# Kernel tuning notes

Measured on AMD Instinct MI355X. Metric: run time of the kernel, lower is better.

## Reference

```python
import jax, jax.numpy as jnp
import numpy as np

N = 50000      # nodes
E = 500000     # edges (includes N self-loops)
DIN = 512
DOUT = 256
NEG_SLOPE = 0.01  # torch nn.LeakyReLU default


def setup_inputs() -> dict:
    key = jax.random.key(0)
    k1, k2, k3, k4, k5 = jax.random.split(key, 5)
    x = jax.random.normal(k1, (N, DIN), dtype=jnp.float32)
    # xavier_normal_ with gain=1.414
    std_W = 1.414 * np.sqrt(2.0 / (DIN + DOUT))
    W = jax.random.normal(k2, (DIN, DOUT), dtype=jnp.float32) * std_W
    std_a = 1.414 * np.sqrt(2.0 / (1 + 2 * DOUT))
    a = jax.random.normal(k3, (2 * DOUT,), dtype=jnp.float32) * std_a
    # first N edges are self-loops so every row-sum is nonzero
    loops = jnp.arange(N, dtype=jnp.int32)
    edge_src = jnp.concatenate([loops, jax.random.randint(k4, (E - N,), 0, N, dtype=jnp.int32)])
    edge_dst = jnp.concatenate([loops, jax.random.randint(k5, (E - N,), 0, N, dtype=jnp.int32)])
    return {"x": x, "W": W, "a": a, "edge_src": edge_src, "edge_dst": edge_dst}


def reference(x, W, a, edge_src, edge_dst):
    n = x.shape[0]
    d = W.shape[1]
    h = x @ W  # [N, DOUT]
    # a . [h_src ; h_dst] decomposed per-node, then gathered per-edge
    s_src = h @ a[:d]   # [N]
    s_dst = h @ a[d:]   # [N]
    score = s_src[edge_src] + s_dst[edge_dst]          # [E]
    e = jnp.exp(-jax.nn.leaky_relu(score, NEG_SLOPE))  # [E]
    # sparse softmax denominator: spmm(edge, e, ones) == segment sum over src
    e_rowsum = jax.ops.segment_sum(e, edge_src, num_segments=n)            # [N]
    # numerator: spmm(edge, e, h) == sum_j e_ij * h_j per row i
    h_prime = jax.ops.segment_sum(e[:, None] * h[edge_dst], edge_src, num_segments=n)  # [N, DOUT]
    h_prime = h_prime / e_rowsum[:, None]
    return jax.nn.elu(h_prime)  # concat=True branch
```

## Files before the change

kernel.cpp:

```cpp
#include <hip/hip_runtime.h>
#include <math.h>

#define DIN 512
#define DOUT 256
#define NEG_SLOPE 0.01f

typedef __attribute__((ext_vector_type(8))) short bf16x8;
typedef __attribute__((ext_vector_type(4))) float f32x4;
typedef __attribute__((ext_vector_type(4))) unsigned int u32x4;

__device__ __forceinline__ unsigned short f2bf(float f) {
    unsigned int u = __float_as_uint(f);
    unsigned int r = (u + 0x7FFFu + ((u >> 16) & 1u)) >> 16;
    return (unsigned short)r;
}
__device__ __forceinline__ float bf2f(unsigned short u) {
    return __uint_as_float(((unsigned int)u) << 16);
}
__device__ __forceinline__ unsigned int cvtpk(float lo, float hi) {
    unsigned int r;
    asm("v_cvt_pk_bf16_f32 %0, %1, %2" : "=v"(r) : "v"(lo), "v"(hi));
    return r;
}
__device__ __forceinline__ void gload16(const void* g, void* l) {
    __builtin_amdgcn_global_load_lds(
        (const __attribute__((address_space(1))) void*)g,
        (__attribute__((address_space(3))) void*)l, 16, 0, 0);
}

__global__ void prep(const float* __restrict__ W, unsigned short* __restrict__ Bp,
                     int* __restrict__ deg, float* __restrict__ s_src,
                     float* __restrict__ s_dst, int N) {
    int t = blockIdx.x * blockDim.x + threadIdx.x;
    if (t < (DIN / 32) * (DOUT / 16) * 64) {
        int lane = t & 63;
        int cg = (t >> 6) & 15;
        int ks = t >> 10;
        int l15 = lane & 15, g = lane >> 4;
        int col = cg * 16 + l15;
        int k0 = ks * 32 + g * 8;
        ushort4 lo, hi;
        lo.x = f2bf(W[(size_t)(k0 + 0) * DOUT + col]);
        lo.y = f2bf(W[(size_t)(k0 + 1) * DOUT + col]);
        lo.z = f2bf(W[(size_t)(k0 + 2) * DOUT + col]);
        lo.w = f2bf(W[(size_t)(k0 + 3) * DOUT + col]);
        hi.x = f2bf(W[(size_t)(k0 + 4) * DOUT + col]);
        hi.y = f2bf(W[(size_t)(k0 + 5) * DOUT + col]);
        hi.z = f2bf(W[(size_t)(k0 + 6) * DOUT + col]);
        hi.w = f2bf(W[(size_t)(k0 + 7) * DOUT + col]);
        *(ushort4*)(Bp + (size_t)t * 8) = lo;
        *(ushort4*)(Bp + (size_t)t * 8 + 4) = hi;
    }
    if (t < N) { deg[t] = 0; s_src[t] = 0.f; s_dst[t] = 0.f; }
}

__global__ __launch_bounds__(64, 3) void gemm_k(const float* __restrict__ x,
                                                const unsigned short* __restrict__ Bp,
                                                unsigned short* __restrict__ hb,
                                                const float* __restrict__ av,
                                                float* __restrict__ s_src,
                                                float* __restrict__ s_dst, int M) {
    __shared__ unsigned char As[16384];
    const int lane = threadIdx.x;
    const int l15 = lane & 15;
    const int g = lane >> 4;
    const int m0 = blockIdx.x * 32;
    const int half = blockIdx.y;

    auto stage = [&](int bb, int ks) {
#pragma unroll
        for (int it = 0; it < 4; ++it) {
            int s = it * 64 + lane;
            int row = s >> 3;
            int slot = s & 7;
            int q = slot ^ (row & 7);
            int rg = min(m0 + row, M - 1);
            const float* src = x + (size_t)rg * DIN + ks * 32 + q * 4;
            gload16(src, As + bb * 4096 + it * 1024);
        }
    };

    const unsigned short* pB = Bp + ((size_t)(half * 8) * 64 + lane) * 8;
    f32x4 acc[2][8] = {};
    bf16x8 bB[2][8];

    stage(0, 0);
    stage(1, 1);
#pragma unroll
    for (int cg = 0; cg < 8; ++cg)
        bB[0][cg] = *(const bf16x8*)(pB + (size_t)cg * 512);

#pragma unroll
    for (int ks = 0; ks < 16; ++ks) {
        if (ks < 14) stage((ks + 2) & 3, ks + 2);
        if (ks < 15) {
            const unsigned short* pBn = pB + (size_t)(ks + 1) * 16 * 512;
#pragma unroll
            for (int cg = 0; cg < 8; ++cg)
                bB[(ks + 1) & 1][cg] = *(const bf16x8*)(pBn + (size_t)cg * 512);
        }
        __builtin_amdgcn_sched_barrier(0);
        if (ks < 14)      asm volatile("s_waitcnt vmcnt(24)");
        else if (ks == 14) asm volatile("s_waitcnt vmcnt(20)");
        else               asm volatile("s_waitcnt vmcnt(16)");
        __builtin_amdgcn_sched_barrier(0);
        const unsigned char* Ab = As + (ks & 3) * 4096;
        const int rr0 = l15, rr1 = l15 + 16;
        f32x4 v0 = *(const f32x4*)(Ab + rr0 * 128 + (((2 * g) ^ (rr0 & 7)) << 4));
        f32x4 v1 = *(const f32x4*)(Ab + rr0 * 128 + (((2 * g + 1) ^ (rr0 & 7)) << 4));
        f32x4 w0 = *(const f32x4*)(Ab + rr1 * 128 + (((2 * g) ^ (rr1 & 7)) << 4));
        f32x4 w1 = *(const f32x4*)(Ab + rr1 * 128 + (((2 * g + 1) ^ (rr1 & 7)) << 4));
        u32x4 p;
        p.x = cvtpk(v0.x, v0.y); p.y = cvtpk(v0.z, v0.w);
        p.z = cvtpk(v1.x, v1.y); p.w = cvtpk(v1.z, v1.w);
        bf16x8 af0 = *(bf16x8*)&p;
        u32x4 q;
        q.x = cvtpk(w0.x, w0.y); q.y = cvtpk(w0.z, w0.w);
        q.z = cvtpk(w1.x, w1.y); q.w = cvtpk(w1.z, w1.w);
        bf16x8 af1 = *(bf16x8*)&q;
#pragma unroll
        for (int cg = 0; cg < 8; ++cg) {
            acc[0][cg] = __builtin_amdgcn_mfma_f32_16x16x32_bf16(af0, bB[ks & 1][cg], acc[0][cg], 0, 0, 0);
            acc[1][cg] = __builtin_amdgcn_mfma_f32_16x16x32_bf16(af1, bB[ks & 1][cg], acc[1][cg], 0, 0, 0);
        }
    }

    float as_[8], ad_[8];
#pragma unroll
    for (int cg = 0; cg < 8; ++cg) {
        int col = half * 128 + cg * 16 + l15;
        as_[cg] = av[col];
        ad_[cg] = av[DOUT + col];
    }
#pragma unroll
    for (int rf = 0; rf < 2; ++rf) {
#pragma unroll
        for (int j = 0; j < 4; ++j) {
            int row = m0 + rf * 16 + g * 4 + j;
            float ps = 0.f, pd = 0.f;
#pragma unroll
            for (int cg = 0; cg < 8; ++cg) {
                float v = acc[rf][cg][j];
                ps += v * as_[cg];
                pd += v * ad_[cg];
            }
#pragma unroll
            for (int off = 1; off < 16; off <<= 1) {
                ps += __shfl_xor(ps, off);
                pd += __shfl_xor(pd, off);
            }
            if (row < M) {
#pragma unroll
                for (int cg = 0; cg < 8; ++cg)
                    hb[(size_t)row * DOUT + half * 128 + cg * 16 + l15] = f2bf(acc[rf][cg][j]);
                if (l15 == 0) {
                    atomicAdd(&s_src[row], ps);
                    atomicAdd(&s_dst[row], pd);
                }
            }
        }
    }
}

__global__ void hist_k(const int* __restrict__ src, int* __restrict__ deg, int E) {
    int i = (blockIdx.x * blockDim.x + threadIdx.x) * 4;
    if (i + 3 < E) {
        int4 v = *(const int4*)(src + i);
        atomicAdd(&deg[v.x], 1);
        atomicAdd(&deg[v.y], 1);
        atomicAdd(&deg[v.z], 1);
        atomicAdd(&deg[v.w], 1);
    } else {
        for (int j = i; j < E; ++j) atomicAdd(&deg[src[j]], 1);
    }
}

__global__ __launch_bounds__(256) void block_sum(const int* __restrict__ deg, int* __restrict__ bsum, int N) {
    __shared__ int wsum[4];
    int b = blockIdx.x, t = threadIdx.x;
    int idx = b * 1024 + t * 4;
    int s = 0;
    if (idx + 3 < N) {
        int4 v = *(const int4*)(deg + idx);
        s = v.x + v.y + v.z + v.w;
    } else {
        for (int i = 0; i < 4; i++) if (idx + i < N) s += deg[idx + i];
    }
#pragma unroll
    for (int off = 32; off > 0; off >>= 1) s += __shfl_xor(s, off);
    if ((t & 63) == 0) wsum[t >> 6] = s;
    __syncthreads();
    if (t == 0) bsum[b] = wsum[0] + wsum[1] + wsum[2] + wsum[3];
}

__global__ __launch_bounds__(256) void scan_blk(const int* __restrict__ deg, const int* __restrict__ bsum,
                                                int* __restrict__ rowptr, int* __restrict__ cursor,
                                                int N, int nb, int E) {
    __shared__ int wsum[4];
    __shared__ int boff_s;
    int b = blockIdx.x, t = threadIdx.x;
    if (t < 64) {
        int v = (t < b && t < nb) ? bsum[t] : 0;
#pragma unroll
        for (int off = 32; off > 0; off >>= 1) v += __shfl_xor(v, off);
        if (t == 0) boff_s = v;
    }
    if (b == 0 && t == 0) rowptr[N] = E;
    int idx = b * 1024 + t * 4;
    int v0 = 0, v1 = 0, v2 = 0, v3 = 0;
    if (idx + 3 < N) {
        int4 v = *(const int4*)(deg + idx);
        v0 = v.x; v1 = v.y; v2 = v.z; v3 = v.w;
    } else if (idx < N) {
        v0 = deg[idx];
        if (idx + 1 < N) v1 = deg[idx + 1];
        if (idx + 2 < N) v2 = deg[idx + 2];
    }
    int s = v0 + v1 + v2 + v3;
    int lane = t & 63, wid = t >> 6;
    int x = s;
#pragma unroll
    for (int off = 1; off < 64; off <<= 1) {
        int y = __shfl_up(x, off);
        if (lane >= off) x += y;
    }
    if (lane == 63) wsum[wid] = x;
    __syncthreads();
    int add = boff_s;
    for (int ww = 0; ww < wid; ++ww) add += wsum[ww];
    int e0 = add + x - s;
    int e1 = e0 + v0, e2 = e1 + v1, e3 = e2 + v2;
    if (idx < N)     { rowptr[idx] = e0;     cursor[idx] = e0; }
    if (idx + 1 < N) { rowptr[idx + 1] = e1; cursor[idx + 1] = e1; }
    if (idx + 2 < N) { rowptr[idx + 2] = e2; cursor[idx + 2] = e2; }
    if (idx + 3 < N) { rowptr[idx + 3] = e3; cursor[idx + 3] = e3; }
}

__global__ void edge_k(const int* __restrict__ src, const int* __restrict__ dst,
                       const float* __restrict__ s_src, const float* __restrict__ s_dst,
                       int* __restrict__ cursor, int2* __restrict__ csr, int E) {
    int i = blockIdx.x * blockDim.x + threadIdx.x;
    if (i >= E) return;
    int s = src[i], d = dst[i];
    float sc = s_src[s] + s_dst[d];
    float lrv = sc > 0.f ? sc : NEG_SLOPE * sc;
    float ev = __expf(-lrv);
    int pos = atomicAdd(&cursor[s], 1);
    csr[pos] = make_int2(d, __float_as_int(ev));
}

__global__ __launch_bounds__(256) void gather_k(const unsigned short* __restrict__ hb,
                                                const int* __restrict__ rowptr,
                                                const int2* __restrict__ csr,
                                                float* __restrict__ out, int N) {
    int gt = blockIdx.x * blockDim.x + threadIdx.x;
    int w = gt >> 6;
    int lane = threadIdx.x & 63;
    if (w >= N) return;
    int s0 = rowptr[w], s1 = rowptr[w + 1];
    float a0 = 0.f, a1 = 0.f, a2 = 0.f, a3 = 0.f, rs = 0.f;
    for (int base = s0; base < s1; base += 64) {
        int cnt = min(64, s1 - base);
        int dv = 0; float ev = 0.f;
        if (lane < cnt) {
            int2 p = csr[base + lane];
            dv = p.x; ev = __int_as_float(p.y);
        }
        int jj = 0;
        for (; jj + 4 <= cnt; jj += 4) {
            int d0 = __shfl(dv, jj), d1 = __shfl(dv, jj + 1), d2 = __shfl(dv, jj + 2), d3 = __shfl(dv, jj + 3);
            float e0 = __shfl(ev, jj), e1 = __shfl(ev, jj + 1), e2 = __shfl(ev, jj + 2), e3 = __shfl(ev, jj + 3);
            ushort4 h0 = *(const ushort4*)(hb + (size_t)d0 * DOUT + lane * 4);
            ushort4 h1 = *(const ushort4*)(hb + (size_t)d1 * DOUT + lane * 4);
            ushort4 h2 = *(const ushort4*)(hb + (size_t)d2 * DOUT + lane * 4);
            ushort4 h3 = *(const ushort4*)(hb + (size_t)d3 * DOUT + lane * 4);
            a0 += e0 * bf2f(h0.x) + e1 * bf2f(h1.x) + e2 * bf2f(h2.x) + e3 * bf2f(h3.x);
            a1 += e0 * bf2f(h0.y) + e1 * bf2f(h1.y) + e2 * bf2f(h2.y) + e3 * bf2f(h3.y);
            a2 += e0 * bf2f(h0.z) + e1 * bf2f(h1.z) + e2 * bf2f(h2.z) + e3 * bf2f(h3.z);
            a3 += e0 * bf2f(h0.w) + e1 * bf2f(h1.w) + e2 * bf2f(h2.w) + e3 * bf2f(h3.w);
            rs += e0 + e1 + e2 + e3;
        }
        for (; jj < cnt; ++jj) {
            int d0 = __shfl(dv, jj);
            float e0 = __shfl(ev, jj);
            ushort4 h0 = *(const ushort4*)(hb + (size_t)d0 * DOUT + lane * 4);
            a0 += e0 * bf2f(h0.x);
            a1 += e0 * bf2f(h0.y);
            a2 += e0 * bf2f(h0.z);
            a3 += e0 * bf2f(h0.w);
            rs += e0;
        }
    }
    float inv = 1.f / rs;
    float4 v;
    v.x = a0 * inv; v.y = a1 * inv; v.z = a2 * inv; v.w = a3 * inv;
    v.x = v.x > 0.f ? v.x : __expf(v.x) - 1.f;
    v.y = v.y > 0.f ? v.y : __expf(v.y) - 1.f;
    v.z = v.z > 0.f ? v.z : __expf(v.z) - 1.f;
    v.w = v.w > 0.f ? v.w : __expf(v.w) - 1.f;
    *(float4*)(out + (size_t)w * DOUT + lane * 4) = v;
}

extern "C" void kernel_launch(void* const* d_in, const int* in_sizes, int n_in,
                              void* d_out, int out_size, void* d_ws, size_t ws_size,
                              hipStream_t stream) {
    const float* x = (const float*)d_in[0];
    const float* W = (const float*)d_in[1];
    const float* a = (const float*)d_in[2];
    const int* edge_src = (const int*)d_in[3];
    const int* edge_dst = (const int*)d_in[4];

    const int N = in_sizes[0] / DIN;
    const int E = in_sizes[3];
    const int nb = (N + 1023) / 1024;

    char* ws = (char*)d_ws;
    size_t off = 0;
    auto alloc = [&](size_t bytes) {
        void* p = ws + off;
        off += (bytes + 15) & ~(size_t)15;
        return p;
    };
    unsigned short* hb = (unsigned short*)alloc((size_t)N * DOUT * 2);
    unsigned short* Bp = (unsigned short*)alloc((size_t)DIN * DOUT * 2);
    int* rowptr = (int*)alloc((size_t)(N + 1) * 4);
    int* deg = (int*)alloc((size_t)N * 4);
    int* cursor = (int*)alloc((size_t)N * 4);
    float* s_src = (float*)alloc((size_t)N * 4);
    float* s_dst = (float*)alloc((size_t)N * 4);
    int2* csr = (int2*)alloc((size_t)E * 8);
    int* bsum = (int*)alloc((size_t)nb * 4);
    (void)ws_size;

    float* out = (float*)d_out;

    prep<<<(N + 255) / 256, 256, 0, stream>>>(W, Bp, deg, s_src, s_dst, N);
    hist_k<<<(E / 4 + 255) / 256, 256, 0, stream>>>(edge_src, deg, E);
    dim3 ggrid((N + 31) / 32, 2);
    gemm_k<<<ggrid, 64, 0, stream>>>(x, Bp, hb, a, s_src, s_dst, N);
    block_sum<<<nb, 256, 0, stream>>>(deg, bsum, N);
    scan_blk<<<nb, 256, 0, stream>>>(deg, bsum, rowptr, cursor, N, nb, E);
    edge_k<<<(E + 255) / 256, 256, 0, stream>>>(edge_src, edge_dst, s_src, s_dst,
                                                cursor, csr, E);
    gather_k<<<(N + 3) / 4, 256, 0, stream>>>(hb, rowptr, csr, out, N);
}
```

Before: 143.5 us.

## Enlarge GEMM row tile to 64, fuse weight prep with degree histogram

The GEMM block now covers 64 rows instead of 32, with four A fragments per K step sharing each B fragment. The A staging drops from four-deep to double buffering, and B is now loaded directly inside the MFMA loop rather than prefetched into registers. Occupancy drops to 2 blocks per SIMD. The weight conversion and edge-source histogram are merged into one kernel, and a single memset now zeroes deg, s_src and s_dst, which were reordered to be contiguous. The aim is fewer launches and more B reuse per A load, at the cost of more register pressure, less latency hiding, and B-load latency exposed in the MFMA loop.

```diff
diff --git a/kernel.cpp b/kernel.cpp
--- a/kernel.cpp
+++ b/kernel.cpp
@@ -28,9 +28,8 @@
         (__attribute__((address_space(3))) void*)l, 16, 0, 0);
 }
 
-__global__ void prep(const float* __restrict__ W, unsigned short* __restrict__ Bp,
-                     int* __restrict__ deg, float* __restrict__ s_src,
-                     float* __restrict__ s_dst, int N) {
+__global__ void prep_hist(const float* __restrict__ W, unsigned short* __restrict__ Bp,
+                          const int* __restrict__ esrc, int* __restrict__ deg, int E) {
     int t = blockIdx.x * blockDim.x + threadIdx.x;
     if (t < (DIN / 32) * (DOUT / 16) * 64) {
         int lane = t & 63;
@@ -51,10 +50,19 @@
         *(ushort4*)(Bp + (size_t)t * 8) = lo;
         *(ushort4*)(Bp + (size_t)t * 8 + 4) = hi;
     }
-    if (t < N) { deg[t] = 0; s_src[t] = 0.f; s_dst[t] = 0.f; }
-}
-
-__global__ __launch_bounds__(64, 3) void gemm_k(const float* __restrict__ x,
+    int i = t * 4;
+    if (i + 3 < E) {
+        int4 v = *(const int4*)(esrc + i);
+        atomicAdd(&deg[v.x], 1);
+        atomicAdd(&deg[v.y], 1);
+        atomicAdd(&deg[v.z], 1);
+        atomicAdd(&deg[v.w], 1);
+    } else {
+        for (int j = i; j < E; ++j) atomicAdd(&deg[esrc[j]], 1);
+    }
+}
+
+__global__ __launch_bounds__(64, 2) void gemm_k(const float* __restrict__ x,
                                                 const unsigned short* __restrict__ Bp,
                                                 unsigned short* __restrict__ hb,
                                                 const float* __restrict__ av,
@@ -64,64 +72,53 @@
     const int lane = threadIdx.x;
     const int l15 = lane & 15;
     const int g = lane >> 4;
-    const int m0 = blockIdx.x * 32;
+    const int m0 = blockIdx.x * 64;
     const int half = blockIdx.y;
 
     auto stage = [&](int bb, int ks) {
 #pragma unroll
-        for (int it = 0; it < 4; ++it) {
+        for (int it = 0; it < 8; ++it) {
             int s = it * 64 + lane;
             int row = s >> 3;
             int slot = s & 7;
             int q = slot ^ (row & 7);
             int rg = min(m0 + row, M - 1);
-            const float* src = x + (size_t)rg * DIN + ks * 32 + q * 4;
-            gload16(src, As + bb * 4096 + it * 1024);
+            gload16(x + (size_t)rg * DIN + ks * 32 + q * 4, As + bb * 8192 + it * 1024);
         }
     };
 
     const unsigned short* pB = Bp + ((size_t)(half * 8) * 64 + lane) * 8;
-    f32x4 acc[2][8] = {};
-    bf16x8 bB[2][8];
+    f32x4 acc[4][8] = {};
 
     stage(0, 0);
-    stage(1, 1);
-#pragma unroll
-    for (int cg = 0; cg < 8; ++cg)
-        bB[0][cg] = *(const bf16x8*)(pB + (size_t)cg * 512);
-
 #pragma unroll
     for (int ks = 0; ks < 16; ++ks) {
-        if (ks < 14) stage((ks + 2) & 3, ks + 2);
+        const int bb = ks & 1;
         if (ks < 15) {
-            const unsigned short* pBn = pB + (size_t)(ks + 1) * 16 * 512;
-#pragma unroll
-            for (int cg = 0; cg < 8; ++cg)
-                bB[(ks + 1) & 1][cg] = *(const bf16x8*)(pBn + (size_t)cg * 512);
-        }
-        __builtin_amdgcn_sched_barrier(0);
-        if (ks < 14)      asm volatile("s_waitcnt vmcnt(24)");
-        else if (ks == 14) asm volatile("s_waitcnt vmcnt(20)");
-        else               asm volatile("s_waitcnt vmcnt(16)");
-        __builtin_amdgcn_sched_barrier(0);
-        const unsigned char* Ab = As + (ks & 3) * 4096;
-        const int rr0 = l15, rr1 = l15 + 16;
-        f32x4 v0 = *(const f32x4*)(Ab + rr0 * 128 + (((2 * g) ^ (rr0 & 7)) << 4));
-        f32x4 v1 = *(const f32x4*)(Ab + rr0 * 128 + (((2 * g + 1) ^ (rr0 & 7)) << 4));
-        f32x4 w0 = *(const f32x4*)(Ab + rr1 * 128 + (((2 * g) ^ (rr1 & 7)) << 4));
-        f32x4 w1 = *(const f32x4*)(Ab + rr1 * 128 + (((2 * g + 1) ^ (rr1 & 7)) << 4));
-        u32x4 p;
-        p.x = cvtpk(v0.x, v0.y); p.y = cvtpk(v0.z, v0.w);
-        p.z = cvtpk(v1.x, v1.y); p.w = cvtpk(v1.z, v1.w);
-        bf16x8 af0 = *(bf16x8*)&p;
-        u32x4 q;
-        q.x = cvtpk(w0.x, w0.y); q.y = cvtpk(w0.z, w0.w);
-        q.z = cvtpk(w1.x, w1.y); q.w = cvtpk(w1.z, w1.w);
-        bf16x8 af1 = *(bf16x8*)&q;
+            stage(bb ^ 1, ks + 1);
+            asm volatile("s_waitcnt vmcnt(8)" ::: "memory");
+        } else {
+            asm volatile("s_waitcnt vmcnt(0)" ::: "memory");
+        }
+        const unsigned char* Ab = As + bb * 8192;
+        bf16x8 af[4];
+#pragma unroll
+        for (int rf = 0; rf < 4; ++rf) {
+            int rr = rf * 16 + l15;
+            f32x4 v0 = *(const f32x4*)(Ab + rr * 128 + (((2 * g) ^ (rr & 7)) << 4));
+            f32x4 v1 = *(const f32x4*)(Ab + rr * 128 + (((2 * g + 1) ^ (rr & 7)) << 4));
+            u32x4 p;
+            p.x = cvtpk(v0.x, v0.y); p.y = cvtpk(v0.z, v0.w);
+            p.z = cvtpk(v1.x, v1.y); p.w = cvtpk(v1.z, v1.w);
+            af[rf] = *(bf16x8*)&p;
+        }
+        const unsigned short* pBks = pB + (size_t)ks * 16 * 512;
 #pragma unroll
         for (int cg = 0; cg < 8; ++cg) {
-            acc[0][cg] = __builtin_amdgcn_mfma_f32_16x16x32_bf16(af0, bB[ks & 1][cg], acc[0][cg], 0, 0, 0);
-            acc[1][cg] = __builtin_amdgcn_mfma_f32_16x16x32_bf16(af1, bB[ks & 1][cg], acc[1][cg], 0, 0, 0);
+            bf16x8 bfr = *(const bf16x8*)(pBks + (size_t)cg * 512);
+#pragma unroll
+            for (int rf = 0; rf < 4; ++rf)
+                acc[rf][cg] = __builtin_amdgcn_mfma_f32_16x16x32_bf16(af[rf], bfr, acc[rf][cg], 0, 0, 0);
         }
     }
 
@@ -133,7 +130,7 @@
         ad_[cg] = av[DOUT + col];
     }
 #pragma unroll
-    for (int rf = 0; rf < 2; ++rf) {
+    for (int rf = 0; rf < 4; ++rf) {
 #pragma unroll
         for (int j = 0; j < 4; ++j) {
             int row = m0 + rf * 16 + g * 4 + j;
@@ -159,19 +156,6 @@
                 }
             }
         }
-    }
-}
-
-__global__ void hist_k(const int* __restrict__ src, int* __restrict__ deg, int E) {
-    int i = (blockIdx.x * blockDim.x + threadIdx.x) * 4;
-    if (i + 3 < E) {
-        int4 v = *(const int4*)(src + i);
-        atomicAdd(&deg[v.x], 1);
-        atomicAdd(&deg[v.y], 1);
-        atomicAdd(&deg[v.z], 1);
-        atomicAdd(&deg[v.w], 1);
-    } else {
-        for (int j = i; j < E; ++j) atomicAdd(&deg[src[j]], 1);
     }
 }
 
@@ -325,18 +309,18 @@
     unsigned short* Bp = (unsigned short*)alloc((size_t)DIN * DOUT * 2);
     int* rowptr = (int*)alloc((size_t)(N + 1) * 4);
     int* deg = (int*)alloc((size_t)N * 4);
-    int* cursor = (int*)alloc((size_t)N * 4);
     float* s_src = (float*)alloc((size_t)N * 4);
     float* s_dst = (float*)alloc((size_t)N * 4);
+    int* cursor = (int*)alloc((size_t)N * 4);
     int2* csr = (int2*)alloc((size_t)E * 8);
     int* bsum = (int*)alloc((size_t)nb * 4);
     (void)ws_size;
 
     float* out = (float*)d_out;
 
-    prep<<<(N + 255) / 256, 256, 0, stream>>>(W, Bp, deg, s_src, s_dst, N);
-    hist_k<<<(E / 4 + 255) / 256, 256, 0, stream>>>(edge_src, deg, E);
-    dim3 ggrid((N + 31) / 32, 2);
+    hipMemsetAsync(deg, 0, (size_t)N * 12, stream);
+    prep_hist<<<(E / 4 + 255) / 256, 256, 0, stream>>>(W, Bp, edge_src, deg, E);
+    dim3 ggrid((N + 63) / 64, 2);
     gemm_k<<<ggrid, 64, 0, stream>>>(x, Bp, hb, a, s_src, s_dst, N);
     block_sum<<<nb, 256, 0, stream>>>(deg, bsum, N);
     scan_blk<<<nb, 256, 0, stream>>>(deg, bsum, rowptr, cursor, N, nb, E);
```

Measured after the change: 147.0 us. +2.5%, slower.
